# Performance work log

Hardware: AMD Instinct MI355X
Metric: run time of the kernel (lower is better)

Reference implementation:

```python
import jax, jax.numpy as jnp
import numpy as np

N_USERS, N_NEWS, N_ENT, N_REL, D, K, NNZ = 10000, 10000, 100000, 32, 64, 20, 500000

def setup_inputs() -> dict:
    key = jax.random.key(0)
    ks = jax.random.split(key, 10)
    return {
        "user_emb": jax.random.normal(ks[0], (N_USERS, D), jnp.float32),
        "news_embeding": jax.random.normal(ks[1], (N_NEWS, D), jnp.float32),
        "entity_emb": jax.random.normal(ks[2], (N_ENT, D), jnp.float32),
        "relation_emb": jax.random.normal(ks[3], (N_REL, D), jnp.float32),
        "news_entities": jax.random.randint(ks[4], (N_NEWS, K), 0, N_ENT),
        "news_relations": jnp.zeros((N_NEWS, K), jnp.int32),  # code forces relation id 0 for news
        "neigh_entities": jax.random.randint(ks[5], (N_ENT, K), 0, N_ENT),
        "neigh_relations": jax.random.randint(ks[6], (N_ENT, K), 0, N_REL),
        "interact_rows": jax.random.randint(ks[7], (NNZ,), 0, N_USERS),
        "interact_cols": jax.random.randint(ks[8], (NNZ,), 0, N_NEWS),
        "interact_vals": jax.random.uniform(ks[9], (NNZ,), jnp.float32),
    }

def _sim_hrt(head, tail, rel):
    # head: [N,D], tail/rel: [N,K,D]
    tail_rel = tail * rel                              # [N,K,D]
    head_rel = head[:, None, :] * rel                  # [N,K,D]
    # NOTE: original norms over the NEIGHBOR dim (dim=1), yielding [N,1,D]
    hnorm = jnp.sqrt(jnp.sum(head_rel * head_rel, axis=1))  # [N,D]
    att = jnp.einsum('nkd,nd->nk', tail_rel, hnorm)    # [N,K]
    return att * att

def _agg(head_emb, neigh_ent_emb, neigh_rel_emb):
    w = jax.nn.softmax(_sim_hrt(head_emb, neigh_ent_emb, neigh_rel_emb), axis=-1)
    return jnp.einsum('nk,nkd->nd', w, neigh_ent_emb)

def reference(user_emb, news_embeding, entity_emb, relation_emb,
              news_entities, news_relations, neigh_entities, neigh_relations,
              interact_rows, interact_cols, interact_vals):
    # news aggregation (newsid = arange -> identity gather on news_embeding)
    news_ne = entity_emb[news_entities]                # [N_news,K,D]
    news_nr = relation_emb[news_relations]             # [N_news,K,D]
    news_agg = _agg(news_embeding, news_ne, news_nr)   # [N_news,D]
    # entity aggregation (entities = arange -> identity gather on entity_emb)
    ent_ne = entity_emb[neigh_entities]                # [N_ent,K,D]
    ent_nr = relation_emb[neigh_relations]             # [N_ent,K,D]
    entity_agg = _agg(entity_emb, ent_ne, ent_nr)      # [N_ent,D]
    # user aggregation: sparse interact_mat @ news_agg via segment_sum
    gathered = interact_vals[:, None] * news_agg[interact_cols]  # [NNZ,D]
    user_agg = jax.ops.segment_sum(gathered, interact_rows, num_segments=N_USERS)
    score = jax.nn.softmax(user_emb @ news_agg.T, axis=-1)       # [N_users,N_news]
    user_agg = user_agg + (score @ news_agg) * user_agg
    return (news_agg, entity_agg, user_agg)
```

## Files before the change

### kernel.cpp

```cpp
#include <hip/hip_runtime.h>
#include <hip/hip_bf16.h>


#define DD 64
#define KK 20
#define NCHUNK 313
#define NSL 20
#define NSTRIP 157
#define NUPAD 10048
#define ATSTRIDE 10016
#define PST32 20

typedef __attribute__((ext_vector_type(8))) short short8;
typedef __attribute__((ext_vector_type(4))) float f32x4;

__device__ __forceinline__ unsigned short f2bf(float x) {
    union { __hip_bfloat16 h; unsigned short u; } cv;
    cv.h = __float2bfloat16(x);
    return cv.u;
}
__device__ __forceinline__ float bfu2f(unsigned short u) {
    return __uint_as_float(((unsigned)u) << 16);
}
#define MFMA16(a, b, c) __builtin_amdgcn_mfma_f32_16x16x32_bf16((a), (b), (c), 0, 0, 0)

__global__ __launch_bounds__(256)
void agg_kernel(const float* __restrict__ head_emb, const float* __restrict__ ent_emb,
                const float* __restrict__ rel_emb,
                const int* __restrict__ ent_idx, const int* __restrict__ rel_idx,
                float* __restrict__ outp, int N)
{
    int w = threadIdx.x >> 6;
    int lane = threadIdx.x & 63;
    int half = lane >> 5;
    int l = lane & 31;
    int n0 = blockIdx.x * 8 + w * 2;
    if (n0 >= N) return;

    float2 head = *(const float2*)(head_emb + (long)(n0 + half) * DD + 2 * l);

    float2 tail[KK], trp[KK];
    float2 s2 = make_float2(0.f, 0.f);
#pragma unroll
    for (int k = 0; k < KK; ++k) {
        int ei0 = ent_idx[n0 * KK + k];
        int ei1 = ent_idx[(n0 + 1) * KK + k];
        int ri0 = rel_idx[n0 * KK + k];
        int ri1 = rel_idx[(n0 + 1) * KK + k];
        int e = half ? ei1 : ei0;
        int r = half ? ri1 : ri0;
        float2 rv = *(const float2*)(rel_emb + (long)r * DD + 2 * l);
        float2 tv = *(const float2*)(ent_emb + (long)e * DD + 2 * l);
        tail[k] = tv;
        trp[k] = make_float2(tv.x * rv.x, tv.y * rv.y);
        s2.x = fmaf(rv.x, rv.x, s2.x);
        s2.y = fmaf(rv.y, rv.y, s2.y);
    }
    float2 hn;
    hn.x = fabsf(head.x) * sqrtf(s2.x);
    hn.y = fabsf(head.y) * sqrtf(s2.y);

    float att[KK];
#pragma unroll
    for (int k = 0; k < KK; ++k) {
        float v = fmaf(trp[k].y, hn.y, trp[k].x * hn.x);
#pragma unroll
        for (int m = 1; m < 32; m <<= 1)
            v += __shfl_xor(v, m, 64);
        att[k] = v * v;
    }
    float mx = att[0];
#pragma unroll
    for (int k = 1; k < KK; ++k) mx = fmaxf(mx, att[k]);
    float den = 0.f;
#pragma unroll
    for (int k = 0; k < KK; ++k) { att[k] = __expf(att[k] - mx); den += att[k]; }
    float inv = 1.f / den;
    float2 o = make_float2(0.f, 0.f);
#pragma unroll
    for (int k = 0; k < KK; ++k) {
        o.x = fmaf(att[k], tail[k].x, o.x);
        o.y = fmaf(att[k], tail[k].y, o.y);
    }
    o.x *= inv; o.y *= inv;
    *(float2*)(outp + (long)(n0 + half) * DD + 2 * l) = o;
}

__global__ __launch_bounds__(256)
void cvt_kernel(const float* __restrict__ src, unsigned short* __restrict__ dst,
                int n_src, int n_total)
{
    int t = blockIdx.x * 256 + threadIdx.x;
    if (t >= n_total) return;
    float v = (t < n_src) ? src[t] : 0.f;
    dst[t] = f2bf(v);
}

__global__ __launch_bounds__(256)
void transpose_kernel(const float* __restrict__ src, unsigned short* __restrict__ AT)
{
    __shared__ float T[128][65];
    int t = threadIdx.x;
    int nb = blockIdx.x * 128;
    const float4* s4 = (const float4*)src;
#pragma unroll
    for (int i = 0; i < 8; ++i) {
        int f = i * 256 + t;
        int row = f >> 4;
        int c4 = f & 15;
        int gr = nb + row;
        float4 v = make_float4(0.f, 0.f, 0.f, 0.f);
        if (gr < 10000) v = s4[(long)gr * 16 + c4];
        T[row][c4 * 4 + 0] = v.x;
        T[row][c4 * 4 + 1] = v.y;
        T[row][c4 * 4 + 2] = v.z;
        T[row][c4 * 4 + 3] = v.w;
    }
    __syncthreads();
    int d = t >> 2;
    int seg = t & 3;
#pragma unroll
    for (int g = 0; g < 8; ++g) {
        int nl = seg * 32 + g * 4;
        int n = nb + nl;
        if (n + 3 < ATSTRIDE) {
            int base = seg * 32;
            ushort4 oh;
            oh.x = f2bf(T[base + 2 * g][d]);
            oh.y = f2bf(T[base + 16 + 2 * g][d]);
            oh.z = f2bf(T[base + 2 * g + 1][d]);
            oh.w = f2bf(T[base + 16 + 2 * g + 1][d]);
            *(ushort4*)(AT + (long)d * ATSTRIDE + n) = oh;
        }
    }
}

__global__ __launch_bounds__(256)
void hist_kernel(const int* __restrict__ rows, int* __restrict__ cnt, int nnz)
{
    int e = blockIdx.x * 256 + threadIdx.x;
    if (e < nnz) atomicAdd(&cnt[rows[e]], 1);
}

__global__ __launch_bounds__(256)
void scan_kernel(const int* __restrict__ cnt, int* __restrict__ offs, int* __restrict__ cur)
{
    __shared__ int ssum[256];
    int t = threadIdx.x;
    int loc[40];
    int s = 0;
#pragma unroll
    for (int i = 0; i < 40; ++i) { loc[i] = s; s += cnt[t * 40 + i]; }
    ssum[t] = s;
    __syncthreads();
    int val = s;
    for (int off = 1; off < 256; off <<= 1) {
        int v = (t >= off) ? ssum[t - off] : 0;
        __syncthreads();
        val += v;
        ssum[t] = val;
        __syncthreads();
    }
    int excl = val - s;
#pragma unroll
    for (int i = 0; i < 40; ++i) {
        int o = excl + loc[i];
        offs[t * 40 + i] = o;
        cur[t * 40 + i] = o;
    }
}

__global__ __launch_bounds__(256)
void fill_kernel(const int* __restrict__ rows, int* __restrict__ cur,
                 int* __restrict__ eid, int nnz)
{
    int e = blockIdx.x * 256 + threadIdx.x;
    if (e < nnz) {
        int p = atomicAdd(&cur[rows[e]], 1);
        eid[p] = e;
    }
}

__global__ __launch_bounds__(256)
void gather_kernel(const int* __restrict__ offs, const int* __restrict__ eid,
                   const int* __restrict__ cols, const float* __restrict__ vals,
                   const float* __restrict__ A, float* __restrict__ seg, int n_users)
{
    int w = threadIdx.x >> 6;
    int lane = threadIdx.x & 63;
    int u = blockIdx.x * 4 + w;
    if (u >= n_users) return;
    int s0 = offs[u], s1 = offs[u + 1];
    float acc = 0.f;
    for (int i = s0; i < s1; ++i) {
        int e = eid[i];
        float v = vals[e];
        int c = cols[e];
        acc = fmaf(v, A[(long)c * DD + lane], acc);
    }
    seg[(long)u * DD + lane] = acc;
}

__global__ __launch_bounds__(256)
void attn_kernel(const unsigned short* __restrict__ Ubf,
                 const unsigned short* __restrict__ Bbf,
                 const unsigned short* __restrict__ ATbf,
                 float* __restrict__ num, float* __restrict__ den)
{
    __shared__ __align__(16) unsigned int Pu[4][2][16 * PST32];

    int w = threadIdx.x >> 6;
    int lane = threadIdx.x & 63;
    int quad = lane >> 4;
    int l15 = lane & 15;
    int wid = blockIdx.x * 4 + w;
    if (wid >= NSTRIP * NSL) return;
    int strip = wid % NSTRIP;
    int slice = wid / NSTRIP;
    int user0 = strip * 64;

    short8 ua0[4], ua1[4];
#pragma unroll
    for (int t = 0; t < 4; ++t) {
        const short* up = (const short*)Ubf + ((long)(user0 + t * 16 + l15)) * 64;
        ua0[t] = *(const short8*)(up + quad * 8);
        ua1[t] = *(const short8*)(up + 32 + quad * 8);
    }

    f32x4 numC[4][4];
    float dena[4][4];
#pragma unroll
    for (int t = 0; t < 4; ++t)
#pragma unroll
        for (int c = 0; c < 4; ++c) {
            numC[t][c] = (f32x4){0.f, 0.f, 0.f, 0.f};
            dena[t][c] = 0.f;
        }

    for (int ch = slice; ch < NCHUNK; ch += NSL) {
        int nb = ch * 32;
        const short* bh = (const short*)Bbf + ((long)(nb + l15)) * 64;
        short8 b00 = *(const short8*)(bh + quad * 8);
        short8 b01 = *(const short8*)(bh + 32 + quad * 8);
        short8 b10 = *(const short8*)(bh + 16 * 64 + quad * 8);
        short8 b11 = *(const short8*)(bh + 16 * 64 + 32 + quad * 8);

        short8 vh[4];
#pragma unroll
        for (int c = 0; c < 4; ++c)
            vh[c] = *(const short8*)((const short*)ATbf +
                    ((long)(16 * c + l15)) * ATSTRIDE + nb + quad * 8);

        bool vlo = (nb + l15) < 10000;
        bool vhi = (nb + 16 + l15) < 10000;
        f32x4 z = {0.f, 0.f, 0.f, 0.f};
#pragma unroll
        for (int p = 0; p < 2; ++p) {
#pragma unroll
            for (int tt = 0; tt < 2; ++tt) {
                int t = p * 2 + tt;
                f32x4 Llo = MFMA16(ua0[t], b00, z);
                Llo = MFMA16(ua1[t], b01, Llo);
                f32x4 Lhi = MFMA16(ua0[t], b10, z);
                Lhi = MFMA16(ua1[t], b11, Lhi);
                unsigned int* Pt = Pu[w][tt];
#pragma unroll
                for (int r = 0; r < 4; ++r) {
                    float plo = vlo ? __expf(fminf(Llo[r], 70.f)) : 0.f;
                    float phi = vhi ? __expf(fminf(Lhi[r], 70.f)) : 0.f;
                    __hip_bfloat162 pk2 = __float22bfloat162_rn(make_float2(plo, phi));
                    unsigned int pk;
                    __builtin_memcpy(&pk, &pk2, 4);
                    Pt[(quad * 4 + r) * PST32 + l15] = pk;
                    dena[t][r] += __uint_as_float(pk << 16)
                                + __uint_as_float(pk & 0xffff0000u);
                }
            }
            short8 ap[2];
#pragma unroll
            for (int tt = 0; tt < 2; ++tt)
                ap[tt] = *(const short8*)((const short*)Pu[w][tt] +
                         l15 * (PST32 * 2) + quad * 8);
#pragma unroll
            for (int c = 0; c < 4; ++c)
#pragma unroll
                for (int tt = 0; tt < 2; ++tt)
                    numC[p * 2 + tt][c] = MFMA16(ap[tt], vh[c], numC[p * 2 + tt][c]);
        }
    }

#pragma unroll
    for (int t = 0; t < 4; ++t)
#pragma unroll
        for (int r = 0; r < 4; ++r) {
#pragma unroll
            for (int m = 1; m < 16; m <<= 1)
                dena[t][r] += __shfl_xor(dena[t][r], m, 64);
        }
    if (l15 == 0) {
#pragma unroll
        for (int t = 0; t < 4; ++t)
#pragma unroll
            for (int r = 0; r < 4; ++r)
                atomicAdd(&den[user0 + t * 16 + quad * 4 + r], dena[t][r]);
    }
#pragma unroll
    for (int t = 0; t < 4; ++t)
#pragma unroll
        for (int c = 0; c < 4; ++c)
#pragma unroll
            for (int r = 0; r < 4; ++r)
                atomicAdd(&num[(long)(user0 + t * 16 + quad * 4 + r) * DD + c * 16 + l15],
                          numC[t][c][r]);
}

__global__ __launch_bounds__(256)
void final_kernel(const float* __restrict__ seg, const float* __restrict__ num,
                  const float* __restrict__ den, float* __restrict__ out, int n_users)
{
    int t = blockIdx.x * 256 + threadIdx.x;
    if (t >= n_users * DD) return;
    int u = t >> 6;
    float s = seg[t];
    float o2 = num[t] / den[u];
    out[t] = fmaf(s, o2, s);
}

extern "C" void kernel_launch(void* const* d_in, const int* in_sizes, int n_in,
                              void* d_out, int out_size, void* d_ws, size_t ws_size,
                              hipStream_t stream)
{
    const float* user_emb = (const float*)d_in[0];
    const float* news_emb = (const float*)d_in[1];
    const float* ent_emb  = (const float*)d_in[2];
    const float* rel_emb  = (const float*)d_in[3];
    const int* news_entities   = (const int*)d_in[4];
    const int* news_relations  = (const int*)d_in[5];
    const int* neigh_entities  = (const int*)d_in[6];
    const int* neigh_relations = (const int*)d_in[7];
    const int* interact_rows   = (const int*)d_in[8];
    const int* interact_cols   = (const int*)d_in[9];
    const float* interact_vals = (const float*)d_in[10];

    const int NU = 10000, NN = 10000, NE = 100000, NNZ = 500000;

    float* out_news = (float*)d_out;
    float* out_ent  = out_news + (long)NN * DD;
    float* out_user = out_ent + (long)NE * DD;

    float* seg  = out_ent;
    float* num  = seg + 640000;
    float* den  = num + 643072;
    int*   cnt  = (int*)(den + 10240);
    int*   offs = cnt + 10240;
    int*   cur  = offs + 10240;
    int*   eid  = cur + 10240;
    unsigned short* Ubf  = (unsigned short*)(eid + 500000);
    unsigned short* Bbf  = Ubf + 643072;
    unsigned short* ATbf = Bbf + 641024;

    hipMemsetAsync(num, 0, (size_t)(643072 + 10240 + 10240) * sizeof(float), stream);

    agg_kernel<<<NN / 8, 256, 0, stream>>>(news_emb, ent_emb, rel_emb,
                                           news_entities, news_relations, out_news, NN);
    cvt_kernel<<<(NUPAD * DD + 255) / 256, 256, 0, stream>>>(user_emb, Ubf, NU * DD, NUPAD * DD);
    cvt_kernel<<<2504, 256, 0, stream>>>(out_news, Bbf, NN * DD, 10016 * DD);
    transpose_kernel<<<(NN + 127) / 128, 256, 0, stream>>>(out_news, ATbf);
    hist_kernel<<<(NNZ + 255) / 256, 256, 0, stream>>>(interact_rows, cnt, NNZ);
    scan_kernel<<<1, 256, 0, stream>>>(cnt, offs, cur);
    fill_kernel<<<(NNZ + 255) / 256, 256, 0, stream>>>(interact_rows, cur, eid, NNZ);
    gather_kernel<<<(NU + 3) / 4, 256, 0, stream>>>(offs, eid, interact_cols,
                                                    interact_vals, out_news, seg, NU);
    attn_kernel<<<(NSTRIP * NSL + 3) / 4, 256, 0, stream>>>(Ubf, Bbf, ATbf, num, den);
    final_kernel<<<(NU * DD + 255) / 256, 256, 0, stream>>>(seg, num, den, out_user, NU);
    agg_kernel<<<NE / 8, 256, 0, stream>>>(ent_emb, ent_emb, rel_emb,
                                           neigh_entities, neigh_relations, out_ent, NE);
}
```

Measured before the change: 464.5 us.

## Fuse attention and entity aggregation into one heterogeneous launch using workspace scratch

Moves the scratch buffers from the entity output region into the provided workspace when it is large enough. That frees the entity aggregation to run alongside the attention kernel, so both are merged into one grid where the first blocks do attention and the rest do entity aggregation. The aim is to overlap the MFMA-heavy attention with the memory-bound gather aggregation and fill idle CUs. The cost is that the fused kernel's register and LDS use is the maximum of the two bodies, which may lower occupancy for the aggregation blocks. If the workspace is too small, it falls back to the old three-kernel sequence.

```diff
diff --git a/kernel.cpp b/kernel.cpp
--- a/kernel.cpp
+++ b/kernel.cpp
@@ -11,6 +11,9 @@
 #define ATSTRIDE 10016
 #define PST32 20
 
+#define ATTN_BLOCKS 785
+#define AGG_ENT_BLOCKS 12500
+
 typedef __attribute__((ext_vector_type(8))) short short8;
 typedef __attribute__((ext_vector_type(4))) float f32x4;
 
@@ -24,18 +27,17 @@
 }
 #define MFMA16(a, b, c) __builtin_amdgcn_mfma_f32_16x16x32_bf16((a), (b), (c), 0, 0, 0)
 
-__global__ __launch_bounds__(256)
-void agg_kernel(const float* __restrict__ head_emb, const float* __restrict__ ent_emb,
-                const float* __restrict__ rel_emb,
-                const int* __restrict__ ent_idx, const int* __restrict__ rel_idx,
-                float* __restrict__ outp, int N)
+__device__ __forceinline__
+void agg_body(const float* __restrict__ head_emb, const float* __restrict__ ent_emb,
+              const float* __restrict__ rel_emb,
+              const int* __restrict__ ent_idx, const int* __restrict__ rel_idx,
+              float* __restrict__ outp, int bid)
 {
     int w = threadIdx.x >> 6;
     int lane = threadIdx.x & 63;
     int half = lane >> 5;
     int l = lane & 31;
-    int n0 = blockIdx.x * 8 + w * 2;
-    if (n0 >= N) return;
+    int n0 = bid * 8 + w * 2;
 
     float2 head = *(const float2*)(head_emb + (long)(n0 + half) * DD + 2 * l);
 
@@ -87,6 +89,17 @@
 }
 
 __global__ __launch_bounds__(256)
+void agg_kernel(const float* __restrict__ head_emb, const float* __restrict__ ent_emb,
+                const float* __restrict__ rel_emb,
+                const int* __restrict__ ent_idx, const int* __restrict__ rel_idx,
+                float* __restrict__ outp, int N)
+{
+    int n0 = blockIdx.x * 8 + (threadIdx.x >> 6) * 2;
+    if (n0 >= N) return;
+    agg_body(head_emb, ent_emb, rel_emb, ent_idx, rel_idx, outp, blockIdx.x);
+}
+
+__global__ __launch_bounds__(256)
 void cvt_kernel(const float* __restrict__ src, unsigned short* __restrict__ dst,
                 int n_src, int n_total)
 {
@@ -201,20 +214,18 @@
     seg[(long)u * DD + lane] = acc;
 }
 
-__global__ __launch_bounds__(256)
-void attn_kernel(const unsigned short* __restrict__ Ubf,
-                 const unsigned short* __restrict__ Bbf,
-                 const unsigned short* __restrict__ ATbf,
-                 float* __restrict__ num, float* __restrict__ den)
-{
-    __shared__ __align__(16) unsigned int Pu[4][2][16 * PST32];
-
+__device__ __forceinline__
+void attn_body(const unsigned short* __restrict__ Ubf,
+               const unsigned short* __restrict__ Bbf,
+               const unsigned short* __restrict__ ATbf,
+               float* __restrict__ num, float* __restrict__ den,
+               unsigned int* __restrict__ PuAll, int bid)
+{
     int w = threadIdx.x >> 6;
     int lane = threadIdx.x & 63;
     int quad = lane >> 4;
     int l15 = lane & 15;
-    int wid = blockIdx.x * 4 + w;
-    if (wid >= NSTRIP * NSL) return;
+    int wid = bid * 4 + w;
     int strip = wid % NSTRIP;
     int slice = wid / NSTRIP;
     int user0 = strip * 64;
@@ -263,7 +274,7 @@
                 Llo = MFMA16(ua1[t], b01, Llo);
                 f32x4 Lhi = MFMA16(ua0[t], b10, z);
                 Lhi = MFMA16(ua1[t], b11, Lhi);
-                unsigned int* Pt = Pu[w][tt];
+                unsigned int* Pt = PuAll + (w * 2 + tt) * (16 * PST32);
 #pragma unroll
                 for (int r = 0; r < 4; ++r) {
                     float plo = vlo ? __expf(fminf(Llo[r], 70.f)) : 0.f;
@@ -279,7 +290,7 @@
             short8 ap[2];
 #pragma unroll
             for (int tt = 0; tt < 2; ++tt)
-                ap[tt] = *(const short8*)((const short*)Pu[w][tt] +
+                ap[tt] = *(const short8*)((const short*)(PuAll + (w * 2 + tt) * (16 * PST32)) +
                          l15 * (PST32 * 2) + quad * 8);
 #pragma unroll
             for (int c = 0; c < 4; ++c)
@@ -312,6 +323,35 @@
             for (int r = 0; r < 4; ++r)
                 atomicAdd(&num[(long)(user0 + t * 16 + quad * 4 + r) * DD + c * 16 + l15],
                           numC[t][c][r]);
+}
+
+__global__ __launch_bounds__(256)
+void attn_kernel(const unsigned short* __restrict__ Ubf,
+                 const unsigned short* __restrict__ Bbf,
+                 const unsigned short* __restrict__ ATbf,
+                 float* __restrict__ num, float* __restrict__ den)
+{
+    __shared__ __align__(16) unsigned int Pu[8][16 * PST32];
+    if (blockIdx.x * 4 + (threadIdx.x >> 6) >= NSTRIP * NSL) return;
+    attn_body(Ubf, Bbf, ATbf, num, den, &Pu[0][0], blockIdx.x);
+}
+
+__global__ __launch_bounds__(256)
+void fused_kernel(const unsigned short* __restrict__ Ubf,
+                  const unsigned short* __restrict__ Bbf,
+                  const unsigned short* __restrict__ ATbf,
+                  float* __restrict__ num, float* __restrict__ den,
+                  const float* __restrict__ ent_emb, const float* __restrict__ rel_emb,
+                  const int* __restrict__ ent_idx, const int* __restrict__ rel_idx,
+                  float* __restrict__ out_ent)
+{
+    __shared__ __align__(16) unsigned int Pu[8][16 * PST32];
+    if (blockIdx.x < ATTN_BLOCKS) {
+        attn_body(Ubf, Bbf, ATbf, num, den, &Pu[0][0], blockIdx.x);
+    } else {
+        agg_body(ent_emb, ent_emb, rel_emb, ent_idx, rel_idx, out_ent,
+                 blockIdx.x - ATTN_BLOCKS);
+    }
 }
 
 __global__ __launch_bounds__(256)
@@ -348,7 +388,15 @@
     float* out_ent  = out_news + (long)NN * DD;
     float* out_user = out_ent + (long)NE * DD;
 
-    float* seg  = out_ent;
+    const size_t SCRATCH_F32 =
+        640000 + 643072 + 10240 + 10240 + 10240 + 10240 + 500000;
+    const size_t SCRATCH_BYTES = SCRATCH_F32 * 4 +
+        (size_t)(643072 + 641024 + 641024) * 2;
+
+    bool use_ws = (d_ws != nullptr) && (ws_size >= SCRATCH_BYTES);
+    float* base = use_ws ? (float*)d_ws : out_ent;
+
+    float* seg  = base;
     float* num  = seg + 640000;
     float* den  = num + 643072;
     int*   cnt  = (int*)(den + 10240);
@@ -371,8 +419,16 @@
     fill_kernel<<<(NNZ + 255) / 256, 256, 0, stream>>>(interact_rows, cur, eid, NNZ);
     gather_kernel<<<(NU + 3) / 4, 256, 0, stream>>>(offs, eid, interact_cols,
                                                     interact_vals, out_news, seg, NU);
-    attn_kernel<<<(NSTRIP * NSL + 3) / 4, 256, 0, stream>>>(Ubf, Bbf, ATbf, num, den);
-    final_kernel<<<(NU * DD + 255) / 256, 256, 0, stream>>>(seg, num, den, out_user, NU);
-    agg_kernel<<<NE / 8, 256, 0, stream>>>(ent_emb, ent_emb, rel_emb,
-                                           neigh_entities, neigh_relations, out_ent, NE);
-}
+
+    if (use_ws) {
+        fused_kernel<<<ATTN_BLOCKS + AGG_ENT_BLOCKS, 256, 0, stream>>>(
+            Ubf, Bbf, ATbf, num, den,
+            ent_emb, rel_emb, neigh_entities, neigh_relations, out_ent);
+        final_kernel<<<(NU * DD + 255) / 256, 256, 0, stream>>>(seg, num, den, out_user, NU);
+    } else {
+        attn_kernel<<<ATTN_BLOCKS, 256, 0, stream>>>(Ubf, Bbf, ATbf, num, den);
+        final_kernel<<<(NU * DD + 255) / 256, 256, 0, stream>>>(seg, num, den, out_user, NU);
+        agg_kernel<<<NE / 8, 256, 0, stream>>>(ent_emb, ent_emb, rel_emb,
+                                               neigh_entities, neigh_relations, out_ent, NE);
+    }
+}
```

New measurement: 456.8 us. Within noise of the previous version (-1.7%).
